# Kernel optimization log

Hardware: AMD Instinct MI355X
Metric: run time of the kernel (lower is better)

## Reference

```python
import jax, jax.numpy as jnp
import numpy as np

N_NODES = 100_000
N_EDGES = 1_600_000
N_FEAT = 11
HIDDEN = 128
N_GRAPHS = 4096


def gcn_conv(x, W, b, row, col, n_nodes):
    # PyG GCNConv (default): add self-loops, symmetric deg^-1/2 norm,
    # out[col] += norm * (x @ W)[row], then + bias.
    xw = x @ W  # [N, H]
    ew = jnp.ones(row.shape[0], dtype=xw.dtype)
    deg = jax.ops.segment_sum(ew, col, num_segments=n_nodes)
    dis = jnp.where(deg > 0, jax.lax.rsqrt(deg), 0.0).astype(xw.dtype)
    norm = dis[row] * dis[col]  # [E+N]
    msg = xw[row] * norm[:, None]  # gather + scale
    out = jax.ops.segment_sum(msg, col, num_segments=n_nodes)  # scatter-add
    return out + b


def setup_inputs() -> dict:
    key = jax.random.key(0)
    ks = jax.random.split(key, 12)
    x = jax.random.normal(ks[0], (N_NODES, N_FEAT), dtype=jnp.float32)
    edge_index = jax.random.randint(ks[1], (2, N_EDGES), 0, N_NODES, dtype=jnp.int64)
    batch = jnp.sort(jax.random.randint(ks[2], (N_NODES,), 0, N_GRAPHS, dtype=jnp.int64))

    def glorot(k, shape):
        lim = float(np.sqrt(6.0 / (shape[0] + shape[1])))
        return jax.random.uniform(k, shape, jnp.float32, -lim, lim)

    W1 = glorot(ks[3], (N_FEAT, HIDDEN))
    b1 = jnp.zeros((HIDDEN,), jnp.float32)
    W2 = glorot(ks[4], (HIDDEN, HIDDEN))
    b2 = jnp.zeros((HIDDEN,), jnp.float32)
    Wl1 = glorot(ks[5], (HIDDEN, HIDDEN))
    bl1 = jnp.zeros((HIDDEN,), jnp.float32)
    Wl2 = glorot(ks[6], (HIDDEN, 1))
    bl2 = jnp.zeros((1,), jnp.float32)
    return {"x": x, "W1": W1, "b1": b1, "W2": W2, "b2": b2,
            "Wl1": Wl1, "bl1": bl1, "Wl2": Wl2, "bl2": bl2,
            "edge_index": edge_index, "batch": batch}


def reference(x, W1, b1, W2, b2, Wl1, bl1, Wl2, bl2, edge_index, batch):
    n = x.shape[0]
    loops = jnp.arange(n, dtype=edge_index.dtype)
    row = jnp.concatenate([edge_index[0], loops])
    col = jnp.concatenate([edge_index[1], loops])

    h = jax.nn.relu(gcn_conv(x, W1, b1, row, col, n))
    h = jax.nn.relu(gcn_conv(h, W2, b2, row, col, n))

    # global_mean_pool over per-node graph ids
    sums = jax.ops.segment_sum(h, batch, num_segments=N_GRAPHS)
    cnts = jax.ops.segment_sum(jnp.ones((n,), h.dtype), batch, num_segments=N_GRAPHS)
    pooled = sums / jnp.maximum(cnts, 1.0)[:, None]  # [G, H]

    out = jax.nn.relu(pooled @ Wl1 + bl1) @ Wl2 + bl2  # [G, 1]
    return out
```

## Files before the change

### kernel.cpp

```cpp
#include <hip/hip_runtime.h>

#define NN 100000
#define NE 1600000
#define NF 11
#define HID 128
#define NG 4096

#define BSH 7
#define BNODES 128
#define NBK 782
#define CAP 3072
#define EPB 4096
#define NBB 391

typedef short bf16x8 __attribute__((ext_vector_type(8)));
typedef float f32x4 __attribute__((ext_vector_type(4)));

__device__ __forceinline__ unsigned short f2bf(float f) {
    unsigned u = __float_as_uint(f);
    return (unsigned short)((u + 0x7FFFu + ((u >> 16) & 1u)) >> 16);
}
__device__ __forceinline__ unsigned packbf(float a, float b) {
    return (unsigned)f2bf(a) | ((unsigned)f2bf(b) << 16);
}
__device__ __forceinline__ float bflo(unsigned v) { return __uint_as_float(v << 16); }
__device__ __forceinline__ float bfhi(unsigned v) { return __uint_as_float(v & 0xFFFF0000u); }
__device__ __forceinline__ bf16x8 as_bf(uint4 u) { union { uint4 a; bf16x8 b; } v; v.a = u; return v.b; }

__global__ __launch_bounds__(256) void k_misc(int* __restrict__ bcur,
                                              const float* __restrict__ W2, unsigned* __restrict__ w2t,
                                              const int* __restrict__ batch, int* __restrict__ gs,
                                              int* __restrict__ startp) {
    int i = blockIdx.x * 256 + threadIdx.x;
    if (i < NBK) bcur[i] = 0;
    if (i < HID * 64) {
        int col = i >> 6, kw = i & 63;
        w2t[col * 64 + kw] = packbf(W2[(2 * kw) * HID + col], W2[(2 * kw + 1) * HID + col]);
    }
    if (i <= NG) {
        int lo = 0, hi = NN;
        while (lo < hi) {
            int mid = (lo + hi) >> 1;
            if (batch[mid] < i) lo = mid + 1; else hi = mid;
        }
        gs[i] = lo;
    }
    if (i == 0) startp[NN] = NE;
}

__global__ __launch_bounds__(256) void k_bucket(const int* __restrict__ row, const int* __restrict__ col,
                                                int* __restrict__ bcur, int* __restrict__ staging) {
    __shared__ int cnt[NBK];
    __shared__ int loc[NBK];
    const int tid = threadIdx.x;
    const int e0 = blockIdx.x * EPB;
    for (int i = tid; i < NBK; i += 256) { cnt[i] = 0; loc[i] = 0; }
    __syncthreads();
    int rb[16]; unsigned pay[16];
#pragma unroll
    for (int j = 0; j < 16; ++j) {
        int e = e0 + j * 256 + tid;
        int c = (e < NE) ? col[e] : -1;
        int r = (e < NE) ? row[e] : 0;
        rb[j] = (c >= 0) ? (c >> BSH) : -1;
        pay[j] = (unsigned)r | ((unsigned)(c & (BNODES - 1)) << 17);
        if (rb[j] >= 0) atomicAdd(&cnt[rb[j]], 1);
    }
    __syncthreads();
    for (int b = tid; b < NBK; b += 256) {
        int c = cnt[b];
        cnt[b] = (c > 0) ? atomicAdd(&bcur[b], c) : 0;
    }
    __syncthreads();
#pragma unroll
    for (int j = 0; j < 16; ++j) {
        if (rb[j] >= 0) {
            int p = cnt[rb[j]] + atomicAdd(&loc[rb[j]], 1);
            staging[rb[j] * CAP + p] = (int)pay[j];
        }
    }
}

__global__ __launch_bounds__(256) void k_hist2s(const int* __restrict__ staging, const int* __restrict__ bcur,
                                                float* __restrict__ dis, int* __restrict__ startp,
                                                int* __restrict__ partial) {
    __shared__ int cnt[BNODES];
    __shared__ int sc[BNODES];
    const int b = blockIdx.x, tid = threadIdx.x;
    if (tid < BNODES) cnt[tid] = 0;
    __syncthreads();
    const int sz = bcur[b];
    const int base = b * CAP;
    for (int i = tid; i < sz; i += 256)
        atomicAdd(&cnt[((unsigned)staging[base + i]) >> 17], 1);
    __syncthreads();
    int v = (tid < BNODES) ? cnt[tid] : 0;
    if (tid < BNODES) sc[tid] = v;
    __syncthreads();
    for (int off = 1; off < BNODES; off <<= 1) {
        int u = (tid < BNODES && tid >= off) ? sc[tid - off] : 0;
        __syncthreads();
        if (tid < BNODES) sc[tid] += u;
        __syncthreads();
    }
    int n = b * BNODES + tid;
    if (tid < BNODES && n < NN) {
        startp[n] = sc[tid] - v;
        dis[n] = rsqrtf((float)(v + 1));
    }
    if (tid == BNODES - 1) partial[b] = sc[BNODES - 1];
}

__global__ __launch_bounds__(1024) void k_scan2(int* __restrict__ partial) {
    __shared__ int sh[1024];
    int t = threadIdx.x;
    int v = (t < NBK) ? partial[t] : 0;
    sh[t] = v; __syncthreads();
    for (int off = 1; off < 1024; off <<= 1) {
        int u = (t >= off) ? sh[t - off] : 0; __syncthreads();
        sh[t] += u; __syncthreads();
    }
    if (t < NBK) partial[t] = sh[t] - v;
}

__global__ __launch_bounds__(256) void k_fillbs(const int* __restrict__ staging, const int* __restrict__ bcur,
                                                const int* __restrict__ partial,
                                                int* __restrict__ startp, int* __restrict__ csr) {
    __shared__ int cur[BNODES];
    const int b = blockIdx.x, tid = threadIdx.x;
    const int bb = partial[b];
    int n = b * BNODES + tid;
    if (tid < BNODES) {
        int sfin = 0;
        if (n < NN) {
            sfin = startp[n] + bb;
            startp[n] = sfin;
        }
        cur[tid] = sfin;
    }
    __syncthreads();
    const int sz = bcur[b];
    const int base = b * CAP;
    for (int i = tid; i < sz; i += 256) {
        unsigned p = (unsigned)staging[base + i];
        int pos = atomicAdd(&cur[p >> 17], 1);
        csr[pos] = (int)(p & 0x1FFFF);
    }
}

__global__ __launch_bounds__(256) void k_xd(const float* __restrict__ x, const float* __restrict__ dis,
                                            unsigned* __restrict__ xd8) {
    const int n = blockIdx.x * 16 + (threadIdx.x >> 4);
    const int lane = threadIdx.x & 15;
    float f = (lane < NF) ? x[(size_t)n * NF + lane] : 0.f;
    f *= dis[n];
    float g = __shfl_down(f, 1, 16);
    if ((lane & 1) == 0 && lane < NF)
        xd8[n * 8 + (lane >> 1)] = packbf(f, g);
}

__global__ __launch_bounds__(256) void k_gat1(const unsigned* __restrict__ xd8,
                                              const int* __restrict__ startp,
                                              const int* __restrict__ csr,
                                              float2* __restrict__ aggf2) {
    const int node = blockIdx.x * 4 + (threadIdx.x >> 6);
    const int lane = threadIdx.x & 63;
    const int g = lane >> 3, f = lane & 7;
    const int s = startp[node], e = startp[node + 1];
    float ax = 0.f, ay = 0.f;
    for (int i = s; i < e; i += 64) {
        int idx = (i + lane < e) ? csr[i + lane] : 0;
        int m = e - i;
#pragma unroll
        for (int t = 0; t < 8; ++t) {
            if (t * 8 >= m) break;
            int ei2 = t * 8 + g;
            int r = __shfl(idx, ei2);
            unsigned v = (ei2 < m && f < 6) ? xd8[r * 8 + f] : 0u;
            ax += bflo(v); ay += bfhi(v);
        }
    }
    ax += __shfl_xor(ax, 8);  ay += __shfl_xor(ay, 8);
    ax += __shfl_xor(ax, 16); ay += __shfl_xor(ay, 16);
    ax += __shfl_xor(ax, 32); ay += __shfl_xor(ay, 32);
    if (g == 0 && f < 6) {
        unsigned sv = xd8[node * 8 + f];
        aggf2[node * 8 + f] = make_float2(ax + bflo(sv), ay + bfhi(sv));
    }
}

__global__ __launch_bounds__(256) void k_l1l2(const float2* __restrict__ aggf2,
                                              const float* __restrict__ W1,
                                              const float* __restrict__ b1,
                                              const unsigned* __restrict__ w2t,
                                              const float* __restrict__ dis,
                                              unsigned* __restrict__ yb) {
    __shared__ float w1s[NF * HID];
    __shared__ float xs[64 * 16];
    __shared__ unsigned h1s[64 * 64];
    const int tid = threadIdx.x;
    const int n0 = blockIdx.x * 64;
    const int wid = tid >> 6, lane = tid & 63;
    const int lr = lane & 15, lk = lane >> 4;
    const int colb = wid * 32;

    for (int i = tid; i < NF * HID; i += 256) w1s[i] = W1[i];
#pragma unroll
    for (int p = 0; p < 2; ++p) {
        int idx = p * 256 + tid;
        int nl = idx >> 3, l = idx & 7;
        int n = n0 + nl;
        float2 v = make_float2(0.f, 0.f);
        if (l < 6 && n < NN) v = aggf2[(size_t)n * 8 + l];
        xs[nl * 16 + 2 * l] = v.x;
        xs[nl * 16 + 2 * l + 1] = v.y;
    }
    const uint4* w4 = (const uint4*)w2t;
    bf16x8 Bf[2][4];
#pragma unroll
    for (int c = 0; c < 2; ++c)
#pragma unroll
        for (int ks = 0; ks < 4; ++ks)
            Bf[c][ks] = as_bf(w4[(colb + c * 16 + lr) * 16 + ks * 4 + lk]);
    __syncthreads();

    const int f2 = tid & 63, sub = tid >> 6;
    float2 bb = ((const float2*)b1)[f2];
    const int jsw = f2 >> 2, ci = f2 & 3;
#pragma unroll
    for (int p = 0; p < 16; ++p) {
        int nl = p * 4 + sub;
        int n = n0 + nl;
        float s0 = 0.f, s1 = 0.f;
#pragma unroll
        for (int k = 0; k < NF; ++k) {
            float xv = xs[nl * 16 + k];
            s0 = fmaf(xv, w1s[k * HID + f2 * 2], s0);
            s1 = fmaf(xv, w1s[k * HID + f2 * 2 + 1], s1);
        }
        float d = (n < NN) ? dis[n] : 0.f;
        float ax = fmaxf(fmaf(s0, d, bb.x), 0.f);
        float ay = fmaxf(fmaf(s1, d, bb.y), 0.f);
        h1s[nl * 64 + ((jsw ^ (nl & 15)) << 2) + ci] = packbf(ax, ay);
    }
    __syncthreads();

    const uint4* h4 = (const uint4*)h1s;
    f32x4 acc[4][2];
#pragma unroll
    for (int r = 0; r < 4; ++r)
#pragma unroll
        for (int c = 0; c < 2; ++c) {
            f32x4 z = {0.f, 0.f, 0.f, 0.f};
            acc[r][c] = z;
        }
#pragma unroll
    for (int ks = 0; ks < 4; ++ks) {
        bf16x8 Af[4];
#pragma unroll
        for (int r = 0; r < 4; ++r)
            Af[r] = as_bf(h4[(r * 16 + lr) * 16 + ((ks * 4 + lk) ^ lr)]);
#pragma unroll
        for (int r = 0; r < 4; ++r)
#pragma unroll
            for (int c = 0; c < 2; ++c)
                acc[r][c] = __builtin_amdgcn_mfma_f32_16x16x32_bf16(Af[r], Bf[c][ks], acc[r][c], 0, 0, 0);
    }
    __syncthreads();

#pragma unroll
    for (int r = 0; r < 4; ++r) {
#pragma unroll
        for (int i = 0; i < 4; ++i) {
            int ndl = r * 16 + lk * 4 + i;
            int nd = n0 + ndl;
            float d = (nd < NN) ? dis[nd] : 0.f;
            int swz = ((r * 4 + lk) & 3) << 3;
#pragma unroll
            for (int c = 0; c < 2; ++c) {
                float v = acc[r][c][i] * d;
                float o = __shfl_xor(v, 1);
                if (!(lane & 1)) {
                    int cu = (colb >> 1) + c * 8 + (lr >> 1);
                    h1s[ndl * 64 + (cu ^ swz)] = packbf(v, o);
                }
            }
        }
    }
    __syncthreads();
    uint4* yb4 = (uint4*)yb;
    const uint4* h1s4 = (const uint4*)h1s;
#pragma unroll
    for (int it = 0; it < 4; ++it) {
        int idx4 = it * 256 + tid;
        int ndl = idx4 >> 4, cu4 = (idx4 & 15) * 4;
        int s = (ndl >> 2) & 3;
        int nd = n0 + ndl;
        if (nd < NN)
            yb4[(size_t)nd * 16 + (idx4 & 15)] = h1s4[(ndl * 64 + (cu4 ^ (s << 3))) >> 2];
    }
}

__global__ __launch_bounds__(256) void k_gather(const unsigned* __restrict__ yb,
                                                const int* __restrict__ startp,
                                                const int* __restrict__ csr_rows,
                                                const float* __restrict__ dis,
                                                const float* __restrict__ b,
                                                unsigned* __restrict__ hb) {
    const int node = blockIdx.x * 4 + (threadIdx.x >> 6);
    const int lane = threadIdx.x & 63;
    int s = startp[node], e = startp[node + 1];
    unsigned sv = yb[node * 64 + lane];
    float ax = bflo(sv), ay = bfhi(sv);
    for (int i = s; i < e; i += 64) {
        int idx = (i + lane < e) ? csr_rows[i + lane] : 0;
        int m = min(64, e - i);
        int j = 0;
        for (; j + 7 < m; j += 8) {
            unsigned v[8];
#pragma unroll
            for (int u = 0; u < 8; ++u) {
                int r = __shfl(idx, j + u);
                v[u] = yb[r * 64 + lane];
            }
#pragma unroll
            for (int u = 0; u < 8; ++u) { ax += bflo(v[u]); ay += bfhi(v[u]); }
        }
        for (; j + 3 < m; j += 4) {
            unsigned v[4];
#pragma unroll
            for (int u = 0; u < 4; ++u) {
                int r = __shfl(idx, j + u);
                v[u] = yb[r * 64 + lane];
            }
#pragma unroll
            for (int u = 0; u < 4; ++u) { ax += bflo(v[u]); ay += bfhi(v[u]); }
        }
        for (; j < m; ++j) {
            int r = __shfl(idx, j);
            unsigned v = yb[r * 64 + lane];
            ax += bflo(v); ay += bfhi(v);
        }
    }
    float d = dis[node];
    float2 bb = ((const float2*)b)[lane];
    ax = fmaxf(fmaf(ax, d, bb.x), 0.f);
    ay = fmaxf(fmaf(ay, d, bb.y), 0.f);
    hb[node * 64 + lane] = packbf(ax, ay);
}

__global__ __launch_bounds__(256) void k_pool(const unsigned* __restrict__ hb, const int* __restrict__ gs,
                                              float* __restrict__ pooled) {
    __shared__ float rx[4][64], ry[4][64];
    const int g = blockIdx.x;
    const int w = threadIdx.x >> 6, lane = threadIdx.x & 63;
    int s = gs[g], e = gs[g + 1];
    float ax = 0.f, ay = 0.f;
    for (int n = s + w; n < e; n += 4) {
        unsigned v = hb[(size_t)n * 64 + lane];
        ax += bflo(v); ay += bfhi(v);
    }
    rx[w][lane] = ax; ry[w][lane] = ay;
    __syncthreads();
    if (w == 0) {
        ax = rx[0][lane] + rx[1][lane] + rx[2][lane] + rx[3][lane];
        ay = ry[0][lane] + ry[1][lane] + ry[2][lane] + ry[3][lane];
        float inv = 1.0f / (float)max(e - s, 1);
        pooled[(size_t)g * HID + lane * 2] = ax * inv;
        pooled[(size_t)g * HID + lane * 2 + 1] = ay * inv;
    }
}

__global__ __launch_bounds__(256) void k_head(const float* __restrict__ pooled,
                                              const float* __restrict__ Wl1, const float* __restrict__ bl1,
                                              const float* __restrict__ Wl2, const float* __restrict__ bl2,
                                              float* __restrict__ out) {
    __shared__ float wl[HID * HID];
    __shared__ float p[2][HID];
    __shared__ float red[4];
    const int tid = threadIdx.x;
    const int f = tid & 127, half = tid >> 7;
    const int w = tid >> 6, lane = tid & 63;
    for (int i = tid; i < HID * HID; i += 256) wl[i] = Wl1[i];
    const float w2f = Wl2[f];
    const float b1f = bl1[f];
    const float b2f = bl2[0];
    const int g0 = blockIdx.x * 16;
    for (int gi = 0; gi < 16; gi += 2) {
        int g = g0 + gi + half;
        p[half][f] = pooled[(size_t)g * HID + f];
        __syncthreads();
        float s = b1f;
#pragma unroll 16
        for (int k = 0; k < HID; ++k) s = fmaf(p[half][k], wl[k * HID + f], s);
        s = fmaxf(s, 0.f) * w2f;
#pragma unroll
        for (int off = 1; off < 64; off <<= 1) s += __shfl_xor(s, off);
        if (lane == 0) red[w] = s;
        __syncthreads();
        if (tid < 2) out[g0 + gi + tid] = red[tid * 2] + red[tid * 2 + 1] + b2f;
        __syncthreads();
    }
}

extern "C" void kernel_launch(void* const* d_in, const int* in_sizes, int n_in,
                              void* d_out, int out_size, void* d_ws, size_t ws_size,
                              hipStream_t stream) {
    const float* x   = (const float*)d_in[0];
    const float* W1  = (const float*)d_in[1];
    const float* b1  = (const float*)d_in[2];
    const float* W2  = (const float*)d_in[3];
    const float* b2  = (const float*)d_in[4];
    const float* Wl1 = (const float*)d_in[5];
    const float* bl1 = (const float*)d_in[6];
    const float* Wl2 = (const float*)d_in[7];
    const float* bl2 = (const float*)d_in[8];
    const int* ei    = (const int*)d_in[9];
    const int* batch = (const int*)d_in[10];
    float* out = (float*)d_out;

    const int* row = ei;
    const int* col = ei + NE;

    char* ws = (char*)d_ws;
    size_t off = 0;
    unsigned* yb   = (unsigned*)(ws + off); off += (size_t)NN * 64 * 4;
    unsigned* hb   = (unsigned*)(ws + off); off += (size_t)NN * 64 * 4;
    unsigned* xd8  = (unsigned*)(ws + off); off += (size_t)NN * 8 * 4;
    float2* aggf2  = (float2*)  (ws + off); off += (size_t)NN * 8 * 8;
    float* dis     = (float*)(ws + off); off += (size_t)NN * 4;
    int*   startp  = (int*)  (ws + off); off += (size_t)(NN + 1) * 4;
    int*   partial = (int*)  (ws + off); off += 1024 * 4;
    int*   csr     = (int*)  (ws + off); off += (size_t)NE * 4;
    int*   gs      = (int*)  (ws + off); off += (size_t)(NG + 1) * 4;
    float* pooled  = (float*)(ws + off); off += (size_t)NG * HID * 4;
    int*   bcur    = (int*)  (ws + off); off += (size_t)NBK * 4;
    unsigned* w2t  = (unsigned*)(ws + off); off += (size_t)HID * 64 * 4;
    int*   staging = (int*)hb;

    k_misc<<<32, 256, 0, stream>>>(bcur, W2, w2t, batch, gs, startp);
    k_bucket<<<NBB, 256, 0, stream>>>(row, col, bcur, staging);
    k_hist2s<<<NBK, 256, 0, stream>>>(staging, bcur, dis, startp, partial);
    k_scan2<<<1, 1024, 0, stream>>>(partial);
    k_fillbs<<<NBK, 256, 0, stream>>>(staging, bcur, partial, startp, csr);

    k_xd<<<NN / 16, 256, 0, stream>>>(x, dis, xd8);
    k_gat1<<<NN / 4, 256, 0, stream>>>(xd8, startp, csr, aggf2);
    k_l1l2<<<(NN + 63) / 64, 256, 0, stream>>>(aggf2, W1, b1, w2t, dis, yb);

    k_gather<<<NN / 4, 256, 0, stream>>>(yb, startp, csr, dis, b2, hb);

    k_pool<<<NG, 256, 0, stream>>>(hb, gs, pooled);
    k_head<<<NG / 16, 256, 0, stream>>>(pooled, Wl1, bl1, Wl2, bl2, out);
}
```

Baseline: 206.2 us.

## Fuse x-scaling into histogram kernel, fuse pooling into head, add nontemporal loads

Computes the dis-scaled, bf16-packed input features inside the degree-histogram kernel and drops the separate k_xd launch. Merges global mean pooling into the MLP head kernel, so the pooled intermediate buffer and one launch go away. Adds nontemporal loads on streaming reads of edges, staging, CSR and aggregates. The fused head runs on only 256 blocks, each reducing its 16 graphs with 2 node-strides, so pooling parallelism drops sharply compared with the old 4096-block pool kernel.

Result: slower. 231.5 us (+12.3%).

```diff
diff --git a/kernel.cpp b/kernel.cpp
--- a/kernel.cpp
+++ b/kernel.cpp
@@ -60,8 +60,8 @@
 #pragma unroll
     for (int j = 0; j < 16; ++j) {
         int e = e0 + j * 256 + tid;
-        int c = (e < NE) ? col[e] : -1;
-        int r = (e < NE) ? row[e] : 0;
+        int c = (e < NE) ? __builtin_nontemporal_load(col + e) : -1;
+        int r = (e < NE) ? __builtin_nontemporal_load(row + e) : 0;
         rb[j] = (c >= 0) ? (c >> BSH) : -1;
         pay[j] = (unsigned)r | ((unsigned)(c & (BNODES - 1)) << 17);
         if (rb[j] >= 0) atomicAdd(&cnt[rb[j]], 1);
@@ -82,8 +82,9 @@
 }
 
 __global__ __launch_bounds__(256) void k_hist2s(const int* __restrict__ staging, const int* __restrict__ bcur,
-                                                float* __restrict__ dis, int* __restrict__ startp,
-                                                int* __restrict__ partial) {
+                                                const float* __restrict__ x,
+                                                float* __restrict__ dis, unsigned* __restrict__ xd8,
+                                                int* __restrict__ startp, int* __restrict__ partial) {
     __shared__ int cnt[BNODES];
     __shared__ int sc[BNODES];
     const int b = blockIdx.x, tid = threadIdx.x;
@@ -106,7 +107,15 @@
     int n = b * BNODES + tid;
     if (tid < BNODES && n < NN) {
         startp[n] = sc[tid] - v;
-        dis[n] = rsqrtf((float)(v + 1));
+        float d = rsqrtf((float)(v + 1));
+        dis[n] = d;
+        const float* xr = x + (size_t)n * NF;
+#pragma unroll
+        for (int u = 0; u < 6; ++u) {
+            float a = xr[2 * u] * d;
+            float bq = (2 * u + 1 < NF) ? xr[2 * u + 1] * d : 0.f;
+            xd8[n * 8 + u] = packbf(a, bq);
+        }
     }
     if (tid == BNODES - 1) partial[b] = sc[BNODES - 1];
 }
@@ -142,21 +151,10 @@
     const int sz = bcur[b];
     const int base = b * CAP;
     for (int i = tid; i < sz; i += 256) {
-        unsigned p = (unsigned)staging[base + i];
+        unsigned p = (unsigned)__builtin_nontemporal_load(staging + base + i);
         int pos = atomicAdd(&cur[p >> 17], 1);
         csr[pos] = (int)(p & 0x1FFFF);
     }
-}
-
-__global__ __launch_bounds__(256) void k_xd(const float* __restrict__ x, const float* __restrict__ dis,
-                                            unsigned* __restrict__ xd8) {
-    const int n = blockIdx.x * 16 + (threadIdx.x >> 4);
-    const int lane = threadIdx.x & 15;
-    float f = (lane < NF) ? x[(size_t)n * NF + lane] : 0.f;
-    f *= dis[n];
-    float g = __shfl_down(f, 1, 16);
-    if ((lane & 1) == 0 && lane < NF)
-        xd8[n * 8 + (lane >> 1)] = packbf(f, g);
 }
 
 __global__ __launch_bounds__(256) void k_gat1(const unsigned* __restrict__ xd8,
@@ -211,7 +209,11 @@
         int nl = idx >> 3, l = idx & 7;
         int n = n0 + nl;
         float2 v = make_float2(0.f, 0.f);
-        if (l < 6 && n < NN) v = aggf2[(size_t)n * 8 + l];
+        if (l < 6 && n < NN) {
+            double dv = __builtin_nontemporal_load((const double*)aggf2 + (size_t)n * 8 + l);
+            union { double d; float2 f; } cv; cv.d = dv;
+            v = cv.f;
+        }
         xs[nl * 16 + 2 * l] = v.x;
         xs[nl * 16 + 2 * l + 1] = v.y;
     }
@@ -309,11 +311,12 @@
                                                 unsigned* __restrict__ hb) {
     const int node = blockIdx.x * 4 + (threadIdx.x >> 6);
     const int lane = threadIdx.x & 63;
-    int s = startp[node], e = startp[node + 1];
+    int s = __builtin_nontemporal_load(startp + node);
+    int e = __builtin_nontemporal_load(startp + node + 1);
     unsigned sv = yb[node * 64 + lane];
     float ax = bflo(sv), ay = bfhi(sv);
     for (int i = s; i < e; i += 64) {
-        int idx = (i + lane < e) ? csr_rows[i + lane] : 0;
+        int idx = (i + lane < e) ? __builtin_nontemporal_load(csr_rows + i + lane) : 0;
         int m = min(64, e - i);
         int j = 0;
         for (; j + 7 < m; j += 8) {
@@ -349,34 +352,13 @@
     hb[node * 64 + lane] = packbf(ax, ay);
 }
 
-__global__ __launch_bounds__(256) void k_pool(const unsigned* __restrict__ hb, const int* __restrict__ gs,
-                                              float* __restrict__ pooled) {
-    __shared__ float rx[4][64], ry[4][64];
-    const int g = blockIdx.x;
-    const int w = threadIdx.x >> 6, lane = threadIdx.x & 63;
-    int s = gs[g], e = gs[g + 1];
-    float ax = 0.f, ay = 0.f;
-    for (int n = s + w; n < e; n += 4) {
-        unsigned v = hb[(size_t)n * 64 + lane];
-        ax += bflo(v); ay += bfhi(v);
-    }
-    rx[w][lane] = ax; ry[w][lane] = ay;
-    __syncthreads();
-    if (w == 0) {
-        ax = rx[0][lane] + rx[1][lane] + rx[2][lane] + rx[3][lane];
-        ay = ry[0][lane] + ry[1][lane] + ry[2][lane] + ry[3][lane];
-        float inv = 1.0f / (float)max(e - s, 1);
-        pooled[(size_t)g * HID + lane * 2] = ax * inv;
-        pooled[(size_t)g * HID + lane * 2 + 1] = ay * inv;
-    }
-}
-
-__global__ __launch_bounds__(256) void k_head(const float* __restrict__ pooled,
-                                              const float* __restrict__ Wl1, const float* __restrict__ bl1,
-                                              const float* __restrict__ Wl2, const float* __restrict__ bl2,
-                                              float* __restrict__ out) {
+__global__ __launch_bounds__(256) void k_headp(const unsigned* __restrict__ hb, const int* __restrict__ gs,
+                                               const float* __restrict__ Wl1, const float* __restrict__ bl1,
+                                               const float* __restrict__ Wl2, const float* __restrict__ bl2,
+                                               float* __restrict__ out) {
     __shared__ float wl[HID * HID];
     __shared__ float p[2][HID];
+    __shared__ float tmp[2][HID];
     __shared__ float red[4];
     const int tid = threadIdx.x;
     const int f = tid & 127, half = tid >> 7;
@@ -385,18 +367,32 @@
     const float w2f = Wl2[f];
     const float b1f = bl1[f];
     const float b2f = bl2[0];
+    const int f2l = f & 63;
+    const int nstr = f >> 6;
     const int g0 = blockIdx.x * 16;
     for (int gi = 0; gi < 16; gi += 2) {
         int g = g0 + gi + half;
-        p[half][f] = pooled[(size_t)g * HID + f];
-        __syncthreads();
-        float s = b1f;
+        int s = gs[g], e = gs[g + 1];
+        float ax = 0.f, ay = 0.f;
+        for (int n = s + nstr; n < e; n += 2) {
+            unsigned v = hb[(size_t)n * 64 + f2l];
+            ax += bflo(v); ay += bfhi(v);
+        }
+        if (nstr) { tmp[half][2 * f2l] = ax; tmp[half][2 * f2l + 1] = ay; }
+        __syncthreads();
+        if (!nstr) {
+            float inv = 1.0f / (float)max(e - s, 1);
+            p[half][2 * f2l]     = (ax + tmp[half][2 * f2l]) * inv;
+            p[half][2 * f2l + 1] = (ay + tmp[half][2 * f2l + 1]) * inv;
+        }
+        __syncthreads();
+        float sacc = b1f;
 #pragma unroll 16
-        for (int k = 0; k < HID; ++k) s = fmaf(p[half][k], wl[k * HID + f], s);
-        s = fmaxf(s, 0.f) * w2f;
-#pragma unroll
-        for (int off = 1; off < 64; off <<= 1) s += __shfl_xor(s, off);
-        if (lane == 0) red[w] = s;
+        for (int k = 0; k < HID; ++k) sacc = fmaf(p[half][k], wl[k * HID + f], sacc);
+        sacc = fmaxf(sacc, 0.f) * w2f;
+#pragma unroll
+        for (int off = 1; off < 64; off <<= 1) sacc += __shfl_xor(sacc, off);
+        if (lane == 0) red[w] = sacc;
         __syncthreads();
         if (tid < 2) out[g0 + gi + tid] = red[tid * 2] + red[tid * 2 + 1] + b2f;
         __syncthreads();
@@ -433,23 +429,20 @@
     int*   partial = (int*)  (ws + off); off += 1024 * 4;
     int*   csr     = (int*)  (ws + off); off += (size_t)NE * 4;
     int*   gs      = (int*)  (ws + off); off += (size_t)(NG + 1) * 4;
-    float* pooled  = (float*)(ws + off); off += (size_t)NG * HID * 4;
     int*   bcur    = (int*)  (ws + off); off += (size_t)NBK * 4;
     unsigned* w2t  = (unsigned*)(ws + off); off += (size_t)HID * 64 * 4;
     int*   staging = (int*)hb;
 
     k_misc<<<32, 256, 0, stream>>>(bcur, W2, w2t, batch, gs, startp);
     k_bucket<<<NBB, 256, 0, stream>>>(row, col, bcur, staging);
-    k_hist2s<<<NBK, 256, 0, stream>>>(staging, bcur, dis, startp, partial);
+    k_hist2s<<<NBK, 256, 0, stream>>>(staging, bcur, x, dis, xd8, startp, partial);
     k_scan2<<<1, 1024, 0, stream>>>(partial);
     k_fillbs<<<NBK, 256, 0, stream>>>(staging, bcur, partial, startp, csr);
 
-    k_xd<<<NN / 16, 256, 0, stream>>>(x, dis, xd8);
     k_gat1<<<NN / 4, 256, 0, stream>>>(xd8, startp, csr, aggf2);
     k_l1l2<<<(NN + 63) / 64, 256, 0, stream>>>(aggf2, W1, b1, w2t, dis, yb);
 
     k_gather<<<NN / 4, 256, 0, stream>>>(yb, startp, csr, dis, b2, hb);
 
-    k_pool<<<NG, 256, 0, stream>>>(hb, gs, pooled);
-    k_head<<<NG / 16, 256, 0, stream>>>(pooled, Wl1, bl1, Wl2, bl2, out);
-}
+    k_headp<<<NG / 16, 256, 0, stream>>>(hb, gs, Wl1, bl1, Wl2, bl2, out);
+}
```
